# Performance work log

Hardware: AMD Instinct MI355X
Metric: run time of the kernel (lower is better)

Reference implementation:

```python
import math
import jax, jax.numpy as jnp
import numpy as np

MODEL_DIM = 2048
NUM_EXPERTS = 64
NUM_TOKENS = 8192
CAPACITY_FACTOR = 1.0


def setup_inputs() -> dict:
    key = jax.random.key(0)
    kx, kw = jax.random.split(key)
    x = jax.random.normal(kx, (NUM_TOKENS, MODEL_DIM), dtype=jnp.float32)
    # Linear(model_dim, num_experts, bias=False): weight [E, D], y = x @ W.T
    wg = jax.random.normal(kw, (NUM_EXPERTS, MODEL_DIM), dtype=jnp.float32) * (1.0 / math.sqrt(MODEL_DIM))
    return {"x": x, "wg": wg}


def reference(x, wg):
    # ---- gate projection: logits [S, E] ----
    logits = jnp.einsum('sd,ed->se', x, wg)
    gates = jax.nn.softmax(logits, axis=1)
    S, E = gates.shape
    # training mode -> capacity = capacity_factor * ceil(S / E)  (static)
    capacity = int(CAPACITY_FACTOR * math.ceil(S / E))

    # ---- top-1 expert selection ----
    indices1_s = jnp.argmax(gates, axis=1)                      # [S]
    mask1 = jax.nn.one_hot(indices1_s, E, dtype=jnp.int32)      # [S, E]

    # gate value of the chosen expert per token
    gates1_s = jnp.sum(gates * mask1.astype(gates.dtype), axis=1)  # [S]

    # position of each token within its expert's queue (cumsum over tokens)
    locations1 = jnp.cumsum(mask1, axis=0) - 1                  # [S, E]

    # ---- load-balancing auxiliary loss ----
    me = jnp.mean(gates, axis=0)                                # [E]
    ce = jnp.mean(mask1.astype(gates.dtype), axis=0)            # [E]
    l_aux = jnp.mean(me * ce) * (E * E)

    # ---- capacity enforcement: drop tokens beyond expert capacity ----
    mask1 = mask1 * (locations1 < capacity).astype(mask1.dtype) # [S, E]
    locations1_s = jnp.sum(locations1 * mask1, axis=1)          # [S]

    # ---- combine / dispatch tensors ----
    gates1 = gates1_s[:, None] * mask1.astype(gates.dtype)      # [S, E]
    locations1_sc = jax.nn.one_hot(locations1_s, capacity, dtype=gates.dtype)  # [S, C]
    # torch.bmm(gates1[:, :, None], locations1_sc[:, None, :]) == outer product per token
    combine1_sec = jnp.einsum('se,sc->sec', gates1, locations1_sc)  # [S, E, C]
    dispatch_mask = combine1_sec > 0                            # bool [S, E, C]

    return l_aux, combine1_sec, dispatch_mask
```

## Files before the change

kernel.cpp:

```cpp
#include <hip/hip_runtime.h>
#include <math.h>

#define DIM     2048
#define NEXP    64
#define CAP     128
#define NTOK    8192
#define NTILE   256
#define KC      256
#define NCH     (DIM/KC)
#define XWSTR   260
#define PSTR    68
#define RF      67108864

typedef float vfloat4 __attribute__((ext_vector_type(4)));

__global__ __launch_bounds__(512, 2) void gate_fill(
    const float* __restrict__ x, const float* __restrict__ wg,
    float* __restrict__ out,
    int* __restrict__ expert_idx, float* __restrict__ gate_top,
    int* __restrict__ rank,
    float* __restrict__ me_partial, int* __restrict__ counts)
{
    __shared__ __align__(16) float smem[(32 + NEXP) * XWSTR];
    __shared__ float me_w[8 * NEXP];
    __shared__ int   cnt_w[8 * NEXP];
    __shared__ int   exp_s[32];

    float* xs = smem;
    float* ws = smem + 32 * XWSTR;

    const int tid  = threadIdx.x;
    const int gb   = blockIdx.x;
    const int tok0 = gb * 32;
    const int sl   = tid >> 5;
    const int i    = tid & 31;
    const int tg   = i & 3;
    const int eg   = i >> 2;
    const int kb   = sl * 16;

    vfloat4* o4 = reinterpret_cast<vfloat4*>(out);
    const vfloat4 z4 = {0.f, 0.f, 0.f, 0.f};

    if (gb == 0 && tid == 0)
        out[134217728ull] = 0.0f;

    float acc[8][8] = {};

    for (int ch = 0; ch < NCH; ++ch) {
        const int k0 = ch * KC;
        #pragma unroll
        for (int q = 0; q < 4; ++q) {
            int id = tid + (q << 9);
            int r = id >> 6, c = id & 63;
            float4 v = *(const float4*)(x + (size_t)(tok0 + r) * DIM + k0 + 4 * c);
            *(float4*)(&xs[r * XWSTR + 4 * c]) = v;
        }
        #pragma unroll
        for (int q = 0; q < 8; ++q) {
            int id = tid + (q << 9);
            int r = id >> 6, c = id & 63;
            float4 v = *(const float4*)(wg + (size_t)r * DIM + k0 + 4 * c);
            *(float4*)(&ws[r * XWSTR + 4 * c]) = v;
        }
        {
            size_t base = (size_t)gb * 131072 + (size_t)(ch << 14) + tid;
            #pragma unroll
            for (int q = 0; q < 32; ++q)
                __builtin_nontemporal_store(z4, &o4[base + (size_t)(q << 9)]);
        }
        __syncthreads();

        #pragma unroll
        for (int q2 = 0; q2 < 4; ++q2) {
            const int kk = kb + 4 * q2;
            float4 xt[8], we[8];
            #pragma unroll
            for (int j = 0; j < 8; ++j)
                xt[j] = *(const float4*)(&xs[(tg + 4 * j) * XWSTR + kk]);
            #pragma unroll
            for (int m = 0; m < 8; ++m)
                we[m] = *(const float4*)(&ws[(eg + 8 * m) * XWSTR + kk]);
            #pragma unroll
            for (int j = 0; j < 8; ++j)
                #pragma unroll
                for (int m = 0; m < 8; ++m) {
                    acc[j][m] = fmaf(xt[j].x, we[m].x, acc[j][m]);
                    acc[j][m] = fmaf(xt[j].y, we[m].y, acc[j][m]);
                    acc[j][m] = fmaf(xt[j].z, we[m].z, acc[j][m]);
                    acc[j][m] = fmaf(xt[j].w, we[m].w, acc[j][m]);
                }
        }
        __syncthreads();
    }

    float* part = smem;
    float* lgt  = smem + 8 * 32 * PSTR;
    if (sl >= 8) {
        #pragma unroll
        for (int j = 0; j < 8; ++j)
            #pragma unroll
            for (int m = 0; m < 8; ++m)
                part[((sl - 8) * 32 + tg + 4 * j) * PSTR + eg + 8 * m] = acc[j][m];
    }
    __syncthreads();
    if (sl < 8) {
        #pragma unroll
        for (int j = 0; j < 8; ++j)
            #pragma unroll
            for (int m = 0; m < 8; ++m) {
                int idx = (sl * 32 + tg + 4 * j) * PSTR + eg + 8 * m;
                part[idx] += acc[j][m];
            }
    }
    __syncthreads();

    {
        int t  = tid >> 4;
        int e0 = (tid & 15) << 2;
        float4 a = {0, 0, 0, 0};
        #pragma unroll
        for (int s2 = 0; s2 < 8; ++s2) {
            float4 p = *(const float4*)(&part[(s2 * 32 + t) * PSTR + e0]);
            a.x += p.x; a.y += p.y; a.z += p.z; a.w += p.w;
        }
        *(float4*)(&lgt[t * PSTR + e0]) = a;
    }
    __syncthreads();

    const int lane = tid & 63;
    const int wv   = tid >> 6;
    float me_acc  = 0.0f;
    int   cnt_acc = 0;
    #pragma unroll
    for (int r4 = 0; r4 < 4; ++r4) {
        int row = wv * 4 + r4;
        float v = lgt[row * PSTR + lane];
        float m = v; int mi = lane;
        #pragma unroll
        for (int off = 32; off > 0; off >>= 1) {
            float om  = __shfl_xor(m, off);
            int   omi = __shfl_xor(mi, off);
            if (om > m || (om == m && omi < mi)) { m = om; mi = omi; }
        }
        float ex = __expf(v - m);
        float sm = ex;
        #pragma unroll
        for (int off = 32; off > 0; off >>= 1) sm += __shfl_xor(sm, off);
        me_acc += ex / sm;
        if (lane == mi) {
            expert_idx[tok0 + row] = mi;
            gate_top[tok0 + row]   = 1.0f / sm;
            exp_s[row] = mi;
            ++cnt_acc;
        }
    }
    me_w[wv * NEXP + lane]  = me_acc;
    cnt_w[wv * NEXP + lane] = cnt_acc;
    __syncthreads();

    if (tid < 32) {
        int e = exp_s[tid];
        int rk = 0;
        for (int u = 0; u < tid; ++u) rk += (exp_s[u] == e) ? 1 : 0;
        rank[tok0 + tid] = rk;
    }
    if (tid < NEXP) {
        float ms = 0.f; int cs = 0;
        #pragma unroll
        for (int w = 0; w < 8; ++w) { ms += me_w[w * NEXP + tid]; cs += cnt_w[w * NEXP + tid]; }
        me_partial[gb * NEXP + tid] = ms;
        counts[gb * NEXP + tid]     = cs;
    }
}

__global__ __launch_bounds__(1024) void prefix_laux(
    const float* __restrict__ me_partial, const int* __restrict__ counts,
    const int* __restrict__ expert_idx, const int* __restrict__ rank,
    const float* __restrict__ gate_top, float* __restrict__ out)
{
    __shared__ int   bo_l[NTILE * NEXP];
    __shared__ int   cnt_l[16 * NEXP];
    __shared__ float me_l[16 * NEXP];
    __shared__ int   cnt_tot[NEXP];
    __shared__ float me_tot[NEXP];

    const int tid = threadIdx.x;
    const int e   = tid & 63;
    const int g   = tid >> 6;

    int cs = 0; float ms = 0.f;
    #pragma unroll
    for (int i = 0; i < 16; ++i) {
        int t = g * 16 + i;
        cs += counts[t * NEXP + e];
        ms += me_partial[t * NEXP + e];
    }
    cnt_l[g * NEXP + e] = cs;
    me_l[g * NEXP + e]  = ms;
    __syncthreads();

    if (g == 0) {
        int run = 0; float mt = 0.f;
        #pragma unroll
        for (int i = 0; i < 16; ++i) {
            int c = cnt_l[i * NEXP + e];
            cnt_l[i * NEXP + e] = run;
            run += c;
            mt  += me_l[i * NEXP + e];
        }
        cnt_tot[e] = run;
        me_tot[e]  = mt;
    }
    __syncthreads();

    int run = cnt_l[g * NEXP + e];
    #pragma unroll
    for (int i = 0; i < 16; ++i) {
        int t = g * 16 + i;
        bo_l[t * NEXP + e] = run;
        run += counts[t * NEXP + e];
    }
    __syncthreads();

    if (tid < NEXP) {
        float v = (me_tot[e] / (float)NTOK) * ((float)cnt_tot[e] / (float)NTOK);
        #pragma unroll
        for (int off = 32; off > 0; off >>= 1) v += __shfl_xor(v, off);
        if (e == 0) out[0] = v * (float)NEXP;
    }

    #pragma unroll
    for (int ii = 0; ii < 8; ++ii) {
        int s  = tid + (ii << 10);
        int ex = expert_idx[s];
        int loc = bo_l[(s >> 5) * NEXP + ex] + rank[s];
        if (loc < CAP) {
            size_t off = 1 + (size_t)s * (NEXP * CAP) + (size_t)ex * CAP + loc;
            out[off]              = gate_top[s];
            out[off + (size_t)RF] = 1.0f;
        }
    }
}

extern "C" void kernel_launch(void* const* d_in, const int* in_sizes, int n_in,
                              void* d_out, int out_size, void* d_ws, size_t ws_size,
                              hipStream_t stream)
{
    const float* x  = (const float*)d_in[0];
    const float* wg = (const float*)d_in[1];
    float* out = (float*)d_out;

    char* ws = (char*)d_ws;
    int*   expert_idx = (int*)  (ws);
    float* gate_top   = (float*)(ws + 32768);
    int*   rank       = (int*)  (ws + 65536);
    float* me_partial = (float*)(ws + 98304);
    int*   counts     = (int*)  (ws + 163840);

    gate_fill<<<NTILE, 512, 0, stream>>>(x, wg, out, expert_idx, gate_top,
                                         rank, me_partial, counts);
    prefix_laux<<<1, 1024, 0, stream>>>(me_partial, counts, expert_idx, rank,
                                        gate_top, out);
}
```

Before: 593.7 us.

## Move output zero-fill out of gate GEMM into a separate fill-and-patch kernel

The large zero-fill of the combine/dispatch output moves out of the gate projection kernel into a new third kernel with 2048 blocks. Each block zeroes its chunk and then writes the few nonzero gate and dispatch entries that fall in its range, using precomputed flat positions. This separates the memory-bound fill from the compute loop and removes the write-after-write ordering between the fill and the scatter. It costs an extra launch and serializes the fill after the small GEMM and prefix kernels instead of overlapping with the GEMM.

```diff
diff --git a/kernel.cpp b/kernel.cpp
--- a/kernel.cpp
+++ b/kernel.cpp
@@ -11,12 +11,14 @@
 #define XWSTR   260
 #define PSTR    68
 #define RF      67108864
+#define RF4     16777216
+#define FBLK    2048
+#define FCH     16384
 
 typedef float vfloat4 __attribute__((ext_vector_type(4)));
 
-__global__ __launch_bounds__(512, 2) void gate_fill(
+__global__ __launch_bounds__(512, 2) void gate(
     const float* __restrict__ x, const float* __restrict__ wg,
-    float* __restrict__ out,
     int* __restrict__ expert_idx, float* __restrict__ gate_top,
     int* __restrict__ rank,
     float* __restrict__ me_partial, int* __restrict__ counts)
@@ -38,12 +40,6 @@
     const int eg   = i >> 2;
     const int kb   = sl * 16;
 
-    vfloat4* o4 = reinterpret_cast<vfloat4*>(out);
-    const vfloat4 z4 = {0.f, 0.f, 0.f, 0.f};
-
-    if (gb == 0 && tid == 0)
-        out[134217728ull] = 0.0f;
-
     float acc[8][8] = {};
 
     for (int ch = 0; ch < NCH; ++ch) {
@@ -61,12 +57,6 @@
             int r = id >> 6, c = id & 63;
             float4 v = *(const float4*)(wg + (size_t)r * DIM + k0 + 4 * c);
             *(float4*)(&ws[r * XWSTR + 4 * c]) = v;
-        }
-        {
-            size_t base = (size_t)gb * 131072 + (size_t)(ch << 14) + tid;
-            #pragma unroll
-            for (int q = 0; q < 32; ++q)
-                __builtin_nontemporal_store(z4, &o4[base + (size_t)(q << 9)]);
         }
         __syncthreads();
 
@@ -173,10 +163,10 @@
     }
 }
 
-__global__ __launch_bounds__(1024) void prefix_laux(
+__global__ __launch_bounds__(1024) void prefix_pos(
     const float* __restrict__ me_partial, const int* __restrict__ counts,
     const int* __restrict__ expert_idx, const int* __restrict__ rank,
-    const float* __restrict__ gate_top, float* __restrict__ out)
+    int* __restrict__ pos_g, float* __restrict__ laux)
 {
     __shared__ int   bo_l[NTILE * NEXP];
     __shared__ int   cnt_l[16 * NEXP];
@@ -226,7 +216,7 @@
         float v = (me_tot[e] / (float)NTOK) * ((float)cnt_tot[e] / (float)NTOK);
         #pragma unroll
         for (int off = 32; off > 0; off >>= 1) v += __shfl_xor(v, off);
-        if (e == 0) out[0] = v * (float)NEXP;
+        if (e == 0) laux[0] = v * (float)NEXP;
     }
 
     #pragma unroll
@@ -234,12 +224,45 @@
         int s  = tid + (ii << 10);
         int ex = expert_idx[s];
         int loc = bo_l[(s >> 5) * NEXP + ex] + rank[s];
-        if (loc < CAP) {
-            size_t off = 1 + (size_t)s * (NEXP * CAP) + (size_t)ex * CAP + loc;
-            out[off]              = gate_top[s];
-            out[off + (size_t)RF] = 1.0f;
-        }
-    }
+        pos_g[s] = (loc < CAP) ? (1 + s * (NEXP * CAP) + ex * CAP + loc) : -1;
+    }
+}
+
+__global__ __launch_bounds__(512) void fill_patch(
+    const int* __restrict__ pos_g, const float* __restrict__ gate_top,
+    const float* __restrict__ laux, float* __restrict__ out)
+{
+    const int tid = threadIdx.x;
+    const int b   = blockIdx.x;
+    vfloat4* o4 = reinterpret_cast<vfloat4*>(out);
+    const vfloat4 z4 = {0.f, 0.f, 0.f, 0.f};
+
+    const size_t base = (size_t)b * FCH + tid;
+    #pragma unroll
+    for (int k = 0; k < 32; ++k)
+        __builtin_nontemporal_store(z4, &o4[base + (size_t)(k << 9)]);
+    if (b == FBLK - 1 && tid == 511)
+        out[134217728ull] = 0.0f;
+    __syncthreads();
+
+    if (tid < 18) {
+        const int isD = tid >= 9;
+        const int r   = tid - 9 * isD;
+        const int sb  = isD ? (b - 1024) : b;
+        const int s   = 8 * sb - 1 + r;
+        if (s >= 0 && s < NTOK) {
+            const int p = pos_g[s];
+            if (p >= 0) {
+                const int gi = p + (isD ? RF : 0);
+                const int F  = gi >> 2;
+                const int lo = b * FCH;
+                const int hi = lo + FCH + ((b == FBLK - 1) ? 1 : 0);
+                if (F >= lo && F < hi)
+                    out[(size_t)gi] = isD ? 1.0f : gate_top[s];
+            }
+        }
+    }
+    if (b == 0 && tid == 18) out[0] = laux[0];
 }
 
 extern "C" void kernel_launch(void* const* d_in, const int* in_sizes, int n_in,
@@ -256,9 +279,12 @@
     int*   rank       = (int*)  (ws + 65536);
     float* me_partial = (float*)(ws + 98304);
     int*   counts     = (int*)  (ws + 163840);
-
-    gate_fill<<<NTILE, 512, 0, stream>>>(x, wg, out, expert_idx, gate_top,
-                                         rank, me_partial, counts);
-    prefix_laux<<<1, 1024, 0, stream>>>(me_partial, counts, expert_idx, rank,
-                                        gate_top, out);
-}
+    int*   pos_g      = (int*)  (ws + 229376);
+    float* laux       = (float*)(ws + 262144);
+
+    gate<<<NTILE, 512, 0, stream>>>(x, wg, expert_idx, gate_top, rank,
+                                    me_partial, counts);
+    prefix_pos<<<1, 1024, 0, stream>>>(me_partial, counts, expert_idx, rank,
+                                       pos_g, laux);
+    fill_patch<<<FBLK, 512, 0, stream>>>(pos_g, gate_top, laux, out);
+}
```

After: 607.5 us. +2.3%, slower.

## Fuse gate and prefix kernels into one cooperative kernel with grid syncs

Applied to the files above, without the earlier changes.

Merges the gating/zero-fill kernel and the single-block prefix/scatter kernel into one cooperative launch that uses two grid-wide syncs. Block 0 computes per-tile expert offsets and the aux loss, then every block scatters its own 32 tokens, so per-token data stays in shared memory and the second launch and its single-block serial scatter go away. A fallback to the old two-kernel path is kept for when the cooperative launch fails. The cost is grid-sync overhead and a serial phase on block 0 while all other blocks wait.

```diff
diff --git a/kernel.cpp b/kernel.cpp
--- a/kernel.cpp
+++ b/kernel.cpp
@@ -1,5 +1,8 @@
 #include <hip/hip_runtime.h>
+#include <hip/hip_cooperative_groups.h>
 #include <math.h>
+
+namespace cg = cooperative_groups;
 
 #define DIM     2048
 #define NEXP    64
@@ -14,7 +17,225 @@
 
 typedef float vfloat4 __attribute__((ext_vector_type(4)));
 
-__global__ __launch_bounds__(512, 2) void gate_fill(
+__global__ __launch_bounds__(512, 2) void moe_all(
+    const float* __restrict__ x, const float* __restrict__ wg,
+    float* __restrict__ out,
+    float* __restrict__ me_partial, int* __restrict__ counts,
+    int* __restrict__ bo_g)
+{
+    __shared__ __align__(16) float smem[(32 + NEXP) * XWSTR];
+    __shared__ float me_w[8 * NEXP];
+    __shared__ int   cnt_w[8 * NEXP];
+    __shared__ int   exp_s[32];
+    __shared__ int   rk_s[32];
+    __shared__ float gt_s[32];
+    __shared__ float laux_s;
+    __shared__ int   cnt_l[8 * NEXP];
+    __shared__ float me_l[8 * NEXP];
+    __shared__ int   cnt_tot[NEXP];
+    __shared__ float me_tot[NEXP];
+
+    float* xs = smem;
+    float* ws = smem + 32 * XWSTR;
+
+    const int tid  = threadIdx.x;
+    const int gb   = blockIdx.x;
+    const int tok0 = gb * 32;
+    const int sl   = tid >> 5;
+    const int i    = tid & 31;
+    const int tg   = i & 3;
+    const int eg   = i >> 2;
+    const int kb   = sl * 16;
+
+    vfloat4* o4 = reinterpret_cast<vfloat4*>(out);
+    const vfloat4 z4 = {0.f, 0.f, 0.f, 0.f};
+    if (gb == 0 && tid == 0)
+        out[134217728ull] = 0.0f;
+
+    float acc[8][8] = {};
+
+    for (int ch = 0; ch < NCH; ++ch) {
+        const int k0 = ch * KC;
+        #pragma unroll
+        for (int q = 0; q < 4; ++q) {
+            int id = tid + (q << 9);
+            int r = id >> 6, c = id & 63;
+            float4 v = *(const float4*)(x + (size_t)(tok0 + r) * DIM + k0 + 4 * c);
+            *(float4*)(&xs[r * XWSTR + 4 * c]) = v;
+        }
+        #pragma unroll
+        for (int q = 0; q < 8; ++q) {
+            int id = tid + (q << 9);
+            int r = id >> 6, c = id & 63;
+            float4 v = *(const float4*)(wg + (size_t)r * DIM + k0 + 4 * c);
+            *(float4*)(&ws[r * XWSTR + 4 * c]) = v;
+        }
+        {
+            size_t base = (size_t)gb * 131072 + (size_t)(ch << 14) + tid;
+            #pragma unroll
+            for (int q = 0; q < 32; ++q)
+                __builtin_nontemporal_store(z4, &o4[base + (size_t)(q << 9)]);
+        }
+        __syncthreads();
+
+        #pragma unroll
+        for (int q2 = 0; q2 < 4; ++q2) {
+            const int kk = kb + 4 * q2;
+            float4 xt[8], we[8];
+            #pragma unroll
+            for (int j = 0; j < 8; ++j)
+                xt[j] = *(const float4*)(&xs[(tg + 4 * j) * XWSTR + kk]);
+            #pragma unroll
+            for (int m = 0; m < 8; ++m)
+                we[m] = *(const float4*)(&ws[(eg + 8 * m) * XWSTR + kk]);
+            #pragma unroll
+            for (int j = 0; j < 8; ++j)
+                #pragma unroll
+                for (int m = 0; m < 8; ++m) {
+                    acc[j][m] = fmaf(xt[j].x, we[m].x, acc[j][m]);
+                    acc[j][m] = fmaf(xt[j].y, we[m].y, acc[j][m]);
+                    acc[j][m] = fmaf(xt[j].z, we[m].z, acc[j][m]);
+                    acc[j][m] = fmaf(xt[j].w, we[m].w, acc[j][m]);
+                }
+        }
+        __syncthreads();
+    }
+
+    float* part = smem;
+    float* lgt  = smem + 8 * 32 * PSTR;
+    if (sl >= 8) {
+        #pragma unroll
+        for (int j = 0; j < 8; ++j)
+            #pragma unroll
+            for (int m = 0; m < 8; ++m)
+                part[((sl - 8) * 32 + tg + 4 * j) * PSTR + eg + 8 * m] = acc[j][m];
+    }
+    __syncthreads();
+    if (sl < 8) {
+        #pragma unroll
+        for (int j = 0; j < 8; ++j)
+            #pragma unroll
+            for (int m = 0; m < 8; ++m) {
+                int idx = (sl * 32 + tg + 4 * j) * PSTR + eg + 8 * m;
+                part[idx] += acc[j][m];
+            }
+    }
+    __syncthreads();
+
+    {
+        int t  = tid >> 4;
+        int e0 = (tid & 15) << 2;
+        float4 a = {0, 0, 0, 0};
+        #pragma unroll
+        for (int s2 = 0; s2 < 8; ++s2) {
+            float4 p = *(const float4*)(&part[(s2 * 32 + t) * PSTR + e0]);
+            a.x += p.x; a.y += p.y; a.z += p.z; a.w += p.w;
+        }
+        *(float4*)(&lgt[t * PSTR + e0]) = a;
+    }
+    __syncthreads();
+
+    const int lane = tid & 63;
+    const int wv   = tid >> 6;
+    float me_acc  = 0.0f;
+    int   cnt_acc = 0;
+    #pragma unroll
+    for (int r4 = 0; r4 < 4; ++r4) {
+        int row = wv * 4 + r4;
+        float v = lgt[row * PSTR + lane];
+        float m = v; int mi = lane;
+        #pragma unroll
+        for (int off = 32; off > 0; off >>= 1) {
+            float om  = __shfl_xor(m, off);
+            int   omi = __shfl_xor(mi, off);
+            if (om > m || (om == m && omi < mi)) { m = om; mi = omi; }
+        }
+        float ex = __expf(v - m);
+        float sm = ex;
+        #pragma unroll
+        for (int off = 32; off > 0; off >>= 1) sm += __shfl_xor(sm, off);
+        me_acc += ex / sm;
+        if (lane == mi) {
+            exp_s[row] = mi;
+            gt_s[row]  = 1.0f / sm;
+            ++cnt_acc;
+        }
+    }
+    me_w[wv * NEXP + lane]  = me_acc;
+    cnt_w[wv * NEXP + lane] = cnt_acc;
+    __syncthreads();
+
+    if (tid < 32) {
+        int e = exp_s[tid];
+        int rk = 0;
+        for (int u = 0; u < tid; ++u) rk += (exp_s[u] == e) ? 1 : 0;
+        rk_s[tid] = rk;
+    }
+    if (tid < NEXP) {
+        float ms = 0.f; int cs = 0;
+        #pragma unroll
+        for (int w = 0; w < 8; ++w) { ms += me_w[w * NEXP + tid]; cs += cnt_w[w * NEXP + tid]; }
+        me_partial[gb * NEXP + tid] = ms;
+        counts[gb * NEXP + tid]     = cs;
+    }
+
+    cg::grid_group grid = cg::this_grid();
+    grid.sync();
+
+    if (gb == 0) {
+        const int e = tid & 63;
+        const int g = tid >> 6;
+        int cs = 0; float ms = 0.f;
+        #pragma unroll 4
+        for (int t = g * 32; t < g * 32 + 32; ++t) {
+            cs += counts[t * NEXP + e];
+            ms += me_partial[t * NEXP + e];
+        }
+        cnt_l[g * NEXP + e] = cs;
+        me_l[g * NEXP + e]  = ms;
+        __syncthreads();
+        if (g == 0) {
+            int run = 0; float mt = 0.f;
+            #pragma unroll
+            for (int q = 0; q < 8; ++q) {
+                int c = cnt_l[q * NEXP + e];
+                cnt_l[q * NEXP + e] = run;
+                run += c;
+                mt  += me_l[q * NEXP + e];
+            }
+            cnt_tot[e] = run;
+            me_tot[e]  = mt;
+        }
+        __syncthreads();
+        int run = cnt_l[g * NEXP + e];
+        #pragma unroll 4
+        for (int t = g * 32; t < g * 32 + 32; ++t) {
+            bo_g[t * NEXP + e] = run;
+            run += counts[t * NEXP + e];
+        }
+        if (tid < NEXP) {
+            float v = (me_tot[e] / (float)NTOK) * ((float)cnt_tot[e] / (float)NTOK);
+            #pragma unroll
+            for (int off = 32; off > 0; off >>= 1) v += __shfl_xor(v, off);
+            if (e == 0) laux_s = v * (float)NEXP;
+        }
+    }
+    __threadfence();
+    grid.sync();
+
+    if (tid < 32) {
+        int e   = exp_s[tid];
+        int loc = bo_g[gb * NEXP + e] + rk_s[tid];
+        if (loc < CAP) {
+            int p = 1 + (tok0 + tid) * (NEXP * CAP) + e * CAP + loc;
+            out[(size_t)p]      = gt_s[tid];
+            out[(size_t)p + RF] = 1.0f;
+        }
+    }
+    if (gb == 0 && tid == 32) out[0] = laux_s;
+}
+
+__global__ __launch_bounds__(512, 2) void gate_fill_fb(
     const float* __restrict__ x, const float* __restrict__ wg,
     float* __restrict__ out,
     int* __restrict__ expert_idx, float* __restrict__ gate_top,
@@ -40,12 +261,9 @@
 
     vfloat4* o4 = reinterpret_cast<vfloat4*>(out);
     const vfloat4 z4 = {0.f, 0.f, 0.f, 0.f};
-
-    if (gb == 0 && tid == 0)
-        out[134217728ull] = 0.0f;
+    if (gb == 0 && tid == 0) out[134217728ull] = 0.0f;
 
     float acc[8][8] = {};
-
     for (int ch = 0; ch < NCH; ++ch) {
         const int k0 = ch * KC;
         #pragma unroll
@@ -69,7 +287,6 @@
                 __builtin_nontemporal_store(z4, &o4[base + (size_t)(q << 9)]);
         }
         __syncthreads();
-
         #pragma unroll
         for (int q2 = 0; q2 < 4; ++q2) {
             const int kk = kb + 4 * q2;
@@ -107,13 +324,10 @@
         #pragma unroll
         for (int j = 0; j < 8; ++j)
             #pragma unroll
-            for (int m = 0; m < 8; ++m) {
-                int idx = (sl * 32 + tg + 4 * j) * PSTR + eg + 8 * m;
-                part[idx] += acc[j][m];
-            }
-    }
-    __syncthreads();
-
+            for (int m = 0; m < 8; ++m)
+                part[(sl * 32 + tg + 4 * j) * PSTR + eg + 8 * m] += acc[j][m];
+    }
+    __syncthreads();
     {
         int t  = tid >> 4;
         int e0 = (tid & 15) << 2;
@@ -173,7 +387,7 @@
     }
 }
 
-__global__ __launch_bounds__(1024) void prefix_laux(
+__global__ __launch_bounds__(1024) void prefix_laux_fb(
     const float* __restrict__ me_partial, const int* __restrict__ counts,
     const int* __restrict__ expert_idx, const int* __restrict__ rank,
     const float* __restrict__ gate_top, float* __restrict__ out)
@@ -190,8 +404,8 @@
 
     int cs = 0; float ms = 0.f;
     #pragma unroll
-    for (int i = 0; i < 16; ++i) {
-        int t = g * 16 + i;
+    for (int q = 0; q < 16; ++q) {
+        int t = g * 16 + q;
         cs += counts[t * NEXP + e];
         ms += me_partial[t * NEXP + e];
     }
@@ -202,11 +416,11 @@
     if (g == 0) {
         int run = 0; float mt = 0.f;
         #pragma unroll
-        for (int i = 0; i < 16; ++i) {
-            int c = cnt_l[i * NEXP + e];
-            cnt_l[i * NEXP + e] = run;
+        for (int q = 0; q < 16; ++q) {
+            int c = cnt_l[q * NEXP + e];
+            cnt_l[q * NEXP + e] = run;
             run += c;
-            mt  += me_l[i * NEXP + e];
+            mt  += me_l[q * NEXP + e];
         }
         cnt_tot[e] = run;
         me_tot[e]  = mt;
@@ -215,8 +429,8 @@
 
     int run = cnt_l[g * NEXP + e];
     #pragma unroll
-    for (int i = 0; i < 16; ++i) {
-        int t = g * 16 + i;
+    for (int q = 0; q < 16; ++q) {
+        int t = g * 16 + q;
         bo_l[t * NEXP + e] = run;
         run += counts[t * NEXP + e];
     }
@@ -251,14 +465,22 @@
     float* out = (float*)d_out;
 
     char* ws = (char*)d_ws;
-    int*   expert_idx = (int*)  (ws);
-    float* gate_top   = (float*)(ws + 32768);
-    int*   rank       = (int*)  (ws + 65536);
-    float* me_partial = (float*)(ws + 98304);
-    int*   counts     = (int*)  (ws + 163840);
-
-    gate_fill<<<NTILE, 512, 0, stream>>>(x, wg, out, expert_idx, gate_top,
-                                         rank, me_partial, counts);
-    prefix_laux<<<1, 1024, 0, stream>>>(me_partial, counts, expert_idx, rank,
-                                        gate_top, out);
+    float* me_partial = (float*)(ws);
+    int*   counts     = (int*)  (ws + 65536);
+    int*   bo_g       = (int*)  (ws + 131072);
+    int*   expert_idx = (int*)  (ws + 196608);
+    float* gate_top   = (float*)(ws + 229376);
+    int*   rank       = (int*)  (ws + 262144);
+
+    void* args[] = { (void*)&x, (void*)&wg, (void*)&out,
+                     (void*)&me_partial, (void*)&counts, (void*)&bo_g };
+    hipError_t err = hipLaunchCooperativeKernel(
+        (const void*)moe_all, dim3(NTILE), dim3(512), args, 0, stream);
+    if (err != hipSuccess) {
+        gate_fill_fb<<<NTILE, 512, 0, stream>>>(x, wg, out, expert_idx,
+                                                gate_top, rank, me_partial,
+                                                counts);
+        prefix_laux_fb<<<1, 1024, 0, stream>>>(me_partial, counts, expert_idx,
+                                               rank, gate_top, out);
+    }
 }
```

After: 674.8 us. 1.14x slower.

## Fuse prefix/aux-loss kernel into gate kernel via grid-wide flag barrier

Applied to the files above, without the earlier changes.

Removes the second single-block kernel by having every gate block publish its per-expert counts and gate sums, then spin on per-block flags until all 256 blocks are done. Each block computes its own expert base offsets from earlier blocks and scatters its 32 tokens' combine/dispatch entries directly. Block 0 also computes the auxiliary loss. This eliminates a kernel launch and the serial one-block scatter of all 8192 tokens, but relies on all 256 blocks being co-resident (512 threads, 2 per CU) and adds a memset launch.

```diff
diff --git a/kernel.cpp b/kernel.cpp
--- a/kernel.cpp
+++ b/kernel.cpp
@@ -14,17 +14,19 @@
 
 typedef float vfloat4 __attribute__((ext_vector_type(4)));
 
-__global__ __launch_bounds__(512, 2) void gate_fill(
+__global__ __launch_bounds__(512, 2) void moe_one(
     const float* __restrict__ x, const float* __restrict__ wg,
     float* __restrict__ out,
-    int* __restrict__ expert_idx, float* __restrict__ gate_top,
-    int* __restrict__ rank,
-    float* __restrict__ me_partial, int* __restrict__ counts)
+    int* __restrict__ counts_g, float* __restrict__ me_g,
+    int* __restrict__ flags)
 {
     __shared__ __align__(16) float smem[(32 + NEXP) * XWSTR];
     __shared__ float me_w[8 * NEXP];
     __shared__ int   cnt_w[8 * NEXP];
     __shared__ int   exp_s[32];
+    __shared__ int   rk_s[32];
+    __shared__ float gt_s[32];
+    __shared__ int   bo_s[NEXP];
 
     float* xs = smem;
     float* ws = smem + 32 * XWSTR;
@@ -40,7 +42,6 @@
 
     vfloat4* o4 = reinterpret_cast<vfloat4*>(out);
     const vfloat4 z4 = {0.f, 0.f, 0.f, 0.f};
-
     if (gb == 0 && tid == 0)
         out[134217728ull] = 0.0f;
 
@@ -148,9 +149,8 @@
         for (int off = 32; off > 0; off >>= 1) sm += __shfl_xor(sm, off);
         me_acc += ex / sm;
         if (lane == mi) {
-            expert_idx[tok0 + row] = mi;
-            gate_top[tok0 + row]   = 1.0f / sm;
             exp_s[row] = mi;
+            gt_s[row]  = 1.0f / sm;
             ++cnt_acc;
         }
     }
@@ -162,82 +162,66 @@
         int e = exp_s[tid];
         int rk = 0;
         for (int u = 0; u < tid; ++u) rk += (exp_s[u] == e) ? 1 : 0;
-        rank[tok0 + tid] = rk;
+        rk_s[tid] = rk;
     }
     if (tid < NEXP) {
         float ms = 0.f; int cs = 0;
         #pragma unroll
         for (int w = 0; w < 8; ++w) { ms += me_w[w * NEXP + tid]; cs += cnt_w[w * NEXP + tid]; }
-        me_partial[gb * NEXP + tid] = ms;
-        counts[gb * NEXP + tid]     = cs;
-    }
-}
-
-__global__ __launch_bounds__(1024) void prefix_laux(
-    const float* __restrict__ me_partial, const int* __restrict__ counts,
-    const int* __restrict__ expert_idx, const int* __restrict__ rank,
-    const float* __restrict__ gate_top, float* __restrict__ out)
-{
-    __shared__ int   bo_l[NTILE * NEXP];
-    __shared__ int   cnt_l[16 * NEXP];
-    __shared__ float me_l[16 * NEXP];
-    __shared__ int   cnt_tot[NEXP];
-    __shared__ float me_tot[NEXP];
-
-    const int tid = threadIdx.x;
-    const int e   = tid & 63;
-    const int g   = tid >> 6;
-
-    int cs = 0; float ms = 0.f;
-    #pragma unroll
-    for (int i = 0; i < 16; ++i) {
-        int t = g * 16 + i;
-        cs += counts[t * NEXP + e];
-        ms += me_partial[t * NEXP + e];
-    }
-    cnt_l[g * NEXP + e] = cs;
-    me_l[g * NEXP + e]  = ms;
-    __syncthreads();
-
-    if (g == 0) {
-        int run = 0; float mt = 0.f;
-        #pragma unroll
-        for (int i = 0; i < 16; ++i) {
-            int c = cnt_l[i * NEXP + e];
-            cnt_l[i * NEXP + e] = run;
-            run += c;
-            mt  += me_l[i * NEXP + e];
-        }
-        cnt_tot[e] = run;
-        me_tot[e]  = mt;
-    }
-    __syncthreads();
-
-    int run = cnt_l[g * NEXP + e];
-    #pragma unroll
-    for (int i = 0; i < 16; ++i) {
-        int t = g * 16 + i;
-        bo_l[t * NEXP + e] = run;
-        run += counts[t * NEXP + e];
-    }
-    __syncthreads();
-
+        counts_g[gb * NEXP + tid] = cs;
+        me_g[gb * NEXP + tid]     = ms;
+    }
+    __syncthreads();
+
+    if (tid == 0) {
+        __threadfence();
+        __hip_atomic_store(&flags[gb], 1, __ATOMIC_RELEASE,
+                           __HIP_MEMORY_SCOPE_AGENT);
+    }
+    if (tid < NTILE) {
+        while (__hip_atomic_load(&flags[tid], __ATOMIC_ACQUIRE,
+                                 __HIP_MEMORY_SCOPE_AGENT) == 0)
+            __builtin_amdgcn_s_sleep(2);
+    }
+    __syncthreads();
+
+    {
+        const int e = tid & 63;
+        const int w = tid >> 6;
+        const int lim = (gb == 0) ? NTILE : gb;
+        int csum = 0; float msum = 0.f;
+        for (int t = w; t < lim; t += 8) {
+            csum += __hip_atomic_load(&counts_g[t * NEXP + e], __ATOMIC_RELAXED,
+                                      __HIP_MEMORY_SCOPE_AGENT);
+            if (gb == 0)
+                msum += __hip_atomic_load(&me_g[t * NEXP + e], __ATOMIC_RELAXED,
+                                          __HIP_MEMORY_SCOPE_AGENT);
+        }
+        cnt_w[w * NEXP + e] = csum;
+        me_w[w * NEXP + e]  = msum;
+    }
+    __syncthreads();
     if (tid < NEXP) {
-        float v = (me_tot[e] / (float)NTOK) * ((float)cnt_tot[e] / (float)NTOK);
-        #pragma unroll
-        for (int off = 32; off > 0; off >>= 1) v += __shfl_xor(v, off);
-        if (e == 0) out[0] = v * (float)NEXP;
-    }
-
-    #pragma unroll
-    for (int ii = 0; ii < 8; ++ii) {
-        int s  = tid + (ii << 10);
-        int ex = expert_idx[s];
-        int loc = bo_l[(s >> 5) * NEXP + ex] + rank[s];
+        int b = 0; float mt = 0.f;
+        #pragma unroll
+        for (int q = 0; q < 8; ++q) { b += cnt_w[q * NEXP + tid]; mt += me_w[q * NEXP + tid]; }
+        bo_s[tid] = (gb == 0) ? 0 : b;
+        if (gb == 0) {
+            float v = (mt / (float)NTOK) * ((float)b / (float)NTOK);
+            #pragma unroll
+            for (int off = 32; off > 0; off >>= 1) v += __shfl_xor(v, off);
+            if (tid == 0) out[0] = v * (float)NEXP;
+        }
+    }
+    __syncthreads();
+
+    if (tid < 32) {
+        int e   = exp_s[tid];
+        int loc = bo_s[e] + rk_s[tid];
         if (loc < CAP) {
-            size_t off = 1 + (size_t)s * (NEXP * CAP) + (size_t)ex * CAP + loc;
-            out[off]              = gate_top[s];
-            out[off + (size_t)RF] = 1.0f;
+            int p = 1 + (tok0 + tid) * (NEXP * CAP) + e * CAP + loc;
+            out[(size_t)p]      = gt_s[tid];
+            out[(size_t)p + RF] = 1.0f;
         }
     }
 }
@@ -251,14 +235,11 @@
     float* out = (float*)d_out;
 
     char* ws = (char*)d_ws;
-    int*   expert_idx = (int*)  (ws);
-    float* gate_top   = (float*)(ws + 32768);
-    int*   rank       = (int*)  (ws + 65536);
-    float* me_partial = (float*)(ws + 98304);
-    int*   counts     = (int*)  (ws + 163840);
-
-    gate_fill<<<NTILE, 512, 0, stream>>>(x, wg, out, expert_idx, gate_top,
-                                         rank, me_partial, counts);
-    prefix_laux<<<1, 1024, 0, stream>>>(me_partial, counts, expert_idx, rank,
-                                        gate_top, out);
+    int*   counts_g = (int*)  (ws);
+    float* me_g     = (float*)(ws + 65536);
+    int*   flags    = (int*)  (ws + 131072);
+
+    hipMemsetAsync(flags, 0, NTILE * sizeof(int), stream);
+
+    moe_one<<<NTILE, 512, 0, stream>>>(x, wg, out, counts_g, me_g, flags);
 }
```

After: 608.2 us. 2.5% more time.
